# Performance work log

Hardware: AMD Instinct MI355X
Metric: run time of the kernel (lower is better)

## Reference

```python
import jax, jax.numpy as jnp
import numpy as np

N_NODES = 3070
N_FEAT = 128
N_OUT = 64
H_SIZE = 50
N_EDGES = 49120
BATCH = 128


def setup_inputs() -> dict:
    key = jax.random.key(0)
    ks = jax.random.split(key, 8)
    x_in = jax.random.normal(ks[0], (BATCH, N_NODES, N_FEAT), dtype=jnp.float32)
    edge_index = jax.random.randint(ks[1], (2, N_EDGES), 0, N_NODES, dtype=jnp.int64)
    edge_weight = jax.random.uniform(ks[2], (N_EDGES,), dtype=jnp.float32)
    W = jax.random.normal(ks[3], (N_FEAT, N_OUT), dtype=jnp.float32) / np.sqrt(N_FEAT)
    b = jnp.zeros((N_OUT,), dtype=jnp.float32)
    W_ih = jax.random.normal(ks[4], (H_SIZE, N_OUT), dtype=jnp.float32) / np.sqrt(N_OUT)
    W_hh = jax.random.normal(ks[5], (H_SIZE, H_SIZE), dtype=jnp.float32) / np.sqrt(H_SIZE)
    b_ih = jnp.zeros((H_SIZE,), dtype=jnp.float32)
    b_hh = jnp.zeros((H_SIZE,), dtype=jnp.float32)
    h0 = jax.random.normal(ks[6], (N_NODES, H_SIZE), dtype=jnp.float32)
    return {"x_in": x_in, "edge_index": edge_index, "edge_weight": edge_weight,
            "W": W, "b": b, "W_ih": W_ih, "W_hh": W_hh, "b_ih": b_ih,
            "b_hh": b_hh, "h0": h0}


def _gcn(x, edge_index, edge_weight, W, b):
    # x: (B, N, F). Vectorized GCNConv over the per-sample python loop.
    n = x.shape[1]
    # vectorized form of the dict-based edge-id remap: rank among unique ids
    uniq = jnp.unique(edge_index, size=n, fill_value=2 ** 30)
    ei = jnp.searchsorted(uniq, edge_index)
    src, dst = ei[0], ei[1]
    # GCNConv default: add self loops with weight 1, symmetric normalization
    loop = jnp.arange(n)
    src = jnp.concatenate([src, loop])
    dst = jnp.concatenate([dst, loop])
    ew = jnp.concatenate([edge_weight, jnp.ones((n,), dtype=x.dtype)])
    deg = jax.ops.segment_sum(ew, dst, num_segments=n)
    dinv = jnp.where(deg > 0, jax.lax.rsqrt(deg), jnp.zeros_like(deg))
    norm = dinv[src] * ew * dinv[dst]                 # (E+N,)
    xw = jnp.einsum('bnf,fo->bno', x, W)              # transform first
    msg = xw[:, src, :] * norm[None, :, None]         # (B, E+N, O)
    out = jnp.zeros_like(xw).at[:, dst, :].add(msg)   # scatter-add to targets
    return out + b


def reference(x_in, edge_index, edge_weight, W, b, W_ih, W_hh, b_ih, b_hh, h0):
    # GCN over all B graph samples (shared fixed graph)
    x = _gcn(x_in, edge_index, edge_weight, W, b)     # (B, N, O)
    # input_horizon==3 -> exactly one horizon step; the torch RNN is seq-first,
    # so seq_len = B (sample dim) and batch = N_NODES, hidden hardcoded 50.
    def step(h, xt):                                   # xt: (N, O), h: (N, H)
        h = jnp.tanh(xt @ W_ih.T + b_ih + h @ W_hh.T + b_hh)
        return h, h
    _, x_out = jax.lax.scan(step, h0, x)               # (B, N, H)
    return x_out
```

## Files before the change

kernel.cpp:

```cpp
#include <hip/hip_runtime.h>

#define NN 3070
#define NF 128
#define NO 64
#define NH 50
#define NC 52
#define NE 49120
#define NB 128
#define MTOT (NB * NN)
#define GCAP 1024
#define NBLK 192
#define GWG (NBLK * NB)
#define GPX (GWG / 8)

__global__ __launch_bounds__(256) void init_kernel(int* __restrict__ zb,
    const float* __restrict__ W, const float* __restrict__ Wih, const float* __restrict__ b,
    const float* __restrict__ bih, const float* __restrict__ bhh,
    float* __restrict__ Wp, float* __restrict__ bp) {
  int blk = blockIdx.x;
  int tid = threadIdx.x;
  if (blk < 48) {
    int i = blk * 256 + tid;
    if (i < 4 * NN) zb[i] = 0;
    return;
  }
  int idx = (blk - 48) * 256 + tid;
  if (idx < 128 * 64) {
    int k = idx >> 6, j = idx & 63;
    float s = 0.f;
    if (j < NH) {
      for (int o = 0; o < NO; ++o) s += W[k * NO + o] * Wih[j * NO + o];
    }
    Wp[k * 64 + j] = s;
  }
  if (idx < NC) {
    float s = 0.f;
    if (idx < NH) {
      for (int o = 0; o < NO; ++o) s += b[o] * Wih[idx * NO + o];
      s += bih[idx] + bhh[idx];
    }
    bp[idx] = s;
  }
}

__global__ __launch_bounds__(256) void mark_kernel(const int* __restrict__ ei, int* __restrict__ mark) {
  int i = blockIdx.x * 256 + threadIdx.x;
  if (i < 2 * NE) mark[ei[i]] = 1;
}

__global__ __launch_bounds__(1024) void exscan_kernel(const int* __restrict__ in, int* __restrict__ out,
                                                      int n, int write_total, int do_dinv,
                                                      const float* __restrict__ degw,
                                                      float* __restrict__ dinv, float* __restrict__ selfn) {
  __shared__ int part[1024];
  int tid = threadIdx.x;
  int base = tid * 3;
  if (do_dinv) {
#pragma unroll
    for (int u = 0; u < 3; ++u) {
      int nd = base + u;
      if (nd < NN) {
        float dg = degw[nd] + 1.0f;
        float di = rsqrtf(dg);
        dinv[nd] = di;
        selfn[nd] = di * di;
      }
    }
  }
  int v0 = (base + 0 < n) ? in[base + 0] : 0;
  int v1 = (base + 1 < n) ? in[base + 1] : 0;
  int v2 = (base + 2 < n) ? in[base + 2] : 0;
  int s = v0 + v1 + v2;
  part[tid] = s;
  __syncthreads();
  for (int off = 1; off < 1024; off <<= 1) {
    int t = (tid >= off) ? part[tid - off] : 0;
    __syncthreads();
    part[tid] += t;
    __syncthreads();
  }
  int run = part[tid] - s;
  if (base + 0 < n) out[base + 0] = run; run += v0;
  if (base + 1 < n) out[base + 1] = run; run += v1;
  if (base + 2 < n) out[base + 2] = run;
  if (write_total && tid == 1023) out[n] = part[1023];
}

__global__ __launch_bounds__(256) void remap_deg_kernel(const int* __restrict__ ei, const float* __restrict__ ew,
    const int* __restrict__ ranks, int* __restrict__ srcr, int* __restrict__ dstr,
    int* __restrict__ degc, float* __restrict__ degw) {
  int e = blockIdx.x * 256 + threadIdx.x;
  if (e >= NE) return;
  int s = ranks[ei[e]];
  int d = ranks[ei[NE + e]];
  srcr[e] = s;
  dstr[e] = d;
  atomicAdd(&degc[d], 1);
  atomicAdd(&degw[d], ew[e]);
}

__global__ __launch_bounds__(256) void csr_fill_kernel(const float* __restrict__ ew, const int* __restrict__ srcr,
    const int* __restrict__ dstr, const int* __restrict__ rowptr, int* __restrict__ cursor,
    const float* __restrict__ dinv, int* __restrict__ csr_src, float* __restrict__ csr_norm) {
  int e = blockIdx.x * 256 + threadIdx.x;
  if (e >= NE) return;
  int d = dstr[e];
  int s = srcr[e];
  int pos = rowptr[d] + atomicAdd(&cursor[d], 1);
  csr_src[pos] = s;
  csr_norm[pos] = dinv[s] * ew[e] * dinv[d];
}

__global__ __launch_bounds__(256, 3) void gemm_kernel(const float* __restrict__ A,
    const float* __restrict__ W, float* __restrict__ out) {
  __shared__ float As[256 * 36];
  __shared__ float Ws[32 * 64];
  int tid = threadIdx.x;
  int row0 = blockIdx.x * 256;
  int rg = tid >> 3;
  int cg = tid & 7;
  int c0 = cg * 8;
  float acc[8][8];
#pragma unroll
  for (int i = 0; i < 8; ++i)
#pragma unroll
    for (int j = 0; j < 8; ++j) acc[i][j] = 0.f;

  for (int kc = 0; kc < 4; ++kc) {
#pragma unroll
    for (int j = 0; j < 8; ++j) {
      int f = tid + 256 * j;
      int r = f >> 3, kq = f & 7;
      float4 v = *(const float4*)&A[(size_t)(row0 + r) * NF + kc * 32 + kq * 4];
      *(float4*)&As[r * 36 + kq * 4] = v;
    }
#pragma unroll
    for (int j = 0; j < 2; ++j) {
      int f = tid + 256 * j;
      int kk = f >> 4, cq = f & 15;
      *(float4*)&Ws[kk * 64 + cq * 4] = *(const float4*)&W[(size_t)(kc * 32 + kk) * 64 + cq * 4];
    }
    __syncthreads();
#pragma unroll 2
    for (int k4 = 0; k4 < 32; k4 += 4) {
      float4 a[8];
#pragma unroll
      for (int i = 0; i < 8; ++i) a[i] = *(const float4*)&As[(rg + 32 * i) * 36 + k4];
#pragma unroll
      for (int m = 0; m < 4; ++m) {
        float4 w0 = *(const float4*)&Ws[(k4 + m) * 64 + c0];
        float4 w1 = *(const float4*)&Ws[(k4 + m) * 64 + c0 + 4];
#pragma unroll
        for (int i = 0; i < 8; ++i) {
          float av = (m == 0) ? a[i].x : (m == 1) ? a[i].y : (m == 2) ? a[i].z : a[i].w;
          acc[i][0] += av * w0.x; acc[i][1] += av * w0.y;
          acc[i][2] += av * w0.z; acc[i][3] += av * w0.w;
          acc[i][4] += av * w1.x; acc[i][5] += av * w1.y;
          acc[i][6] += av * w1.z; acc[i][7] += av * w1.w;
        }
      }
    }
    __syncthreads();
  }
#pragma unroll
  for (int i = 0; i < 8; ++i) {
    size_t r = row0 + rg + 32 * i;
    if (c0 < NC)
      *(float4*)&out[r * NC + c0] = make_float4(acc[i][0], acc[i][1], acc[i][2], acc[i][3]);
    if (c0 + 4 < NC)
      *(float4*)&out[r * NC + c0 + 4] = make_float4(acc[i][4], acc[i][5], acc[i][6], acc[i][7]);
  }
}

__global__ __launch_bounds__(256) void gather_kernel(const float4* __restrict__ xw,
    const int* __restrict__ rowptr, const int* __restrict__ csr_src, const float* __restrict__ csr_norm,
    const float* __restrict__ selfn, const float* __restrict__ bp, float4* __restrict__ outg) {
  __shared__ int s_src[GCAP];
  __shared__ float s_nrm[GCAP];
  int bid = blockIdx.x;
  int xcd = bid & 7;
  int pos = bid >> 3;
  int work = xcd * GPX + pos;
  int b = work / NBLK;
  int nblk = work - b * NBLK;
  int tid = threadIdx.x;
  int f4 = tid & 15, nl = tid >> 4;
  int nb = nblk * 16;
  int nend = nb + 16 < NN ? nb + 16 : NN;
  int be0 = rowptr[nb], be1 = rowptr[nend];
  int cnt = be1 - be0;
  int scnt = cnt < GCAP ? cnt : GCAP;
  for (int i = tid; i < scnt; i += 256) {
    s_src[i] = csr_src[be0 + i];
    s_nrm[i] = csr_norm[be0 + i];
  }
  __syncthreads();
  int n = nb + nl;
  if (n >= NN || f4 >= 13) return;
  const float4* xb = xw + (size_t)b * NN * 13;
  float sn = selfn[n];
  float4 v = xb[n * 13 + f4];
  float ax = v.x * sn, ay = v.y * sn, az = v.z * sn, aw = v.w * sn;
  float bx = 0.f, by = 0.f, bz = 0.f, bw = 0.f;
  int le0 = rowptr[n] - be0, le1 = rowptr[n + 1] - be0;
  int lim = le1 < GCAP ? le1 : GCAP;
  int e = le0;
  for (; e + 1 < lim; e += 2) {
    int s1 = s_src[e], s2 = s_src[e + 1];
    float w1 = s_nrm[e], w2 = s_nrm[e + 1];
    float4 u1 = xb[s1 * 13 + f4];
    float4 u2 = xb[s2 * 13 + f4];
    ax += w1 * u1.x; ay += w1 * u1.y; az += w1 * u1.z; aw += w1 * u1.w;
    bx += w2 * u2.x; by += w2 * u2.y; bz += w2 * u2.z; bw += w2 * u2.w;
  }
  if (e < lim) {
    int s1 = s_src[e];
    float w1 = s_nrm[e];
    float4 u1 = xb[s1 * 13 + f4];
    ax += w1 * u1.x; ay += w1 * u1.y; az += w1 * u1.z; aw += w1 * u1.w;
  }
  for (e = (le0 > GCAP ? le0 : GCAP); e < le1; ++e) {
    int s1 = csr_src[be0 + e];
    float w1 = csr_norm[be0 + e];
    float4 u1 = xb[s1 * 13 + f4];
    ax += w1 * u1.x; ay += w1 * u1.y; az += w1 * u1.z; aw += w1 * u1.w;
  }
  float4 bb = ((const float4*)bp)[f4];
  float4 o = make_float4(ax + bx + bb.x, ay + by + bb.y, az + bz + bb.z, aw + bw + bb.w);
  outg[((size_t)b * NN + n) * 13 + f4] = o;
}

__global__ __launch_bounds__(256, 3) void rnn_kernel(const float* __restrict__ pre,
    const float* __restrict__ Whh, const float* __restrict__ h0, float* __restrict__ out) {
  __shared__ float hs[2][6 * 52];
  int tid = threadIdx.x;
  int n0 = blockIdx.x * 5;
  int nl = tid / 50;
  int j = tid - nl * 50;
  bool active = tid < 250;
  int jj = active ? j : 0;
  float2 whh2[25];
  const float2* whhp = (const float2*)(Whh + jj * NH);
#pragma unroll
  for (int q = 0; q < 25; ++q) whh2[q] = whhp[q];
  for (int i = tid; i < 2 * 6 * 52; i += 256) ((float*)hs)[i] = 0.f;
  __syncthreads();
  if (active) hs[0][nl * 52 + j] = h0[n0 * 50 + tid];
  const size_t NPRE = (size_t)NN * NC;
  const size_t NOUT = (size_t)NN * NH;
  int nn = active ? (n0 + nl) : n0;
  const float* prep = pre + (size_t)nn * NC + jj;
  float xp0 = prep[0];
  float xp1 = prep[NPRE];
  int widx = active ? (nl * 52 + j) : (5 * 52 + (tid - 250));
  __syncthreads();
#pragma unroll 2
  for (int t = 0; t < NB; ++t) {
    float a0 = xp0, a1 = 0.f, a2 = 0.f, a3 = 0.f;
    xp0 = xp1;
    if (t + 2 < NB) xp1 = prep[(size_t)(t + 2) * NPRE];
    const float* hb = hs[t & 1];
    const float4* hr = (const float4*)&hb[nl * 52];
#pragma unroll
    for (int q = 0; q < 12; q += 4) {
      float4 h0v = hr[q], h1v = hr[q + 1], h2v = hr[q + 2], h3v = hr[q + 3];
      a0 += h0v.x * whh2[2*q].x   + h0v.y * whh2[2*q].y   + h0v.z * whh2[2*q+1].x + h0v.w * whh2[2*q+1].y;
      a1 += h1v.x * whh2[2*q+2].x + h1v.y * whh2[2*q+2].y + h1v.z * whh2[2*q+3].x + h1v.w * whh2[2*q+3].y;
      a2 += h2v.x * whh2[2*q+4].x + h2v.y * whh2[2*q+4].y + h2v.z * whh2[2*q+5].x + h2v.w * whh2[2*q+5].y;
      a3 += h3v.x * whh2[2*q+6].x + h3v.y * whh2[2*q+6].y + h3v.z * whh2[2*q+7].x + h3v.w * whh2[2*q+7].y;
    }
    {
      float2 ht = *(const float2*)&hb[nl * 52 + 48];
      a0 += ht.x * whh2[24].x + ht.y * whh2[24].y;
    }
    float v = (a0 + a1) + (a2 + a3);
    float e = __expf(-2.f * fabsf(v));
    float r = (1.f - e) * __builtin_amdgcn_rcpf(1.f + e);
    float hnew = (v < 0.f) ? -r : r;
    hs[(t + 1) & 1][widx] = hnew;
    if (active) out[(size_t)t * NOUT + n0 * 50 + tid] = hnew;
    asm volatile("s_waitcnt lgkmcnt(0)" ::: "memory");
    __builtin_amdgcn_s_barrier();
  }
}


extern "C" void kernel_launch(void* const* d_in, const int* in_sizes, int n_in,
                              void* d_out, int out_size, void* d_ws, size_t ws_size,
                              hipStream_t stream) {
  const float* x_in = (const float*)d_in[0];
  const int* ei     = (const int*)d_in[1];
  const float* ew   = (const float*)d_in[2];
  const float* W    = (const float*)d_in[3];
  const float* bias = (const float*)d_in[4];
  const float* Wih  = (const float*)d_in[5];
  const float* Whh  = (const float*)d_in[6];
  const float* bih  = (const float*)d_in[7];
  const float* bhh  = (const float*)d_in[8];
  const float* h0   = (const float*)d_in[9];
  float* out = (float*)d_out;

  char* ws = (char*)d_ws;
  size_t off = 0;
  auto alloc = [&](size_t bytes) {
    size_t o = off;
    off += (bytes + 255) & ~(size_t)255;
    return o;
  };
  float* xw    = (float*)(ws + alloc((size_t)MTOT * NC * 4));
  float* gcn   = (float*)(ws + alloc((size_t)MTOT * NC * 4));
  int*   zb    = (int*)(ws + alloc((size_t)4 * NN * 4));
  int* mark = zb;
  int* degc = zb + NN;
  float* degw = (float*)(zb + 2 * NN);
  int* cursor = zb + 3 * NN;
  int*   ranks  = (int*)(ws + alloc(NN * 4));
  int*   srcr   = (int*)(ws + alloc(NE * 4));
  int*   dstr   = (int*)(ws + alloc(NE * 4));
  float* dinv   = (float*)(ws + alloc(NN * 4));
  float* selfn  = (float*)(ws + alloc(NN * 4));
  int*   rowptr = (int*)(ws + alloc((NN + 1) * 4));
  int*   csrc   = (int*)(ws + alloc(NE * 4));
  float* cnorm  = (float*)(ws + alloc(NE * 4));
  float* Wp     = (float*)(ws + alloc(128 * 64 * 4));
  float* bp     = (float*)(ws + alloc(NC * 4));

  init_kernel<<<80, 256, 0, stream>>>(zb, W, Wih, bias, bih, bhh, Wp, bp);
  mark_kernel<<<(2 * NE + 255) / 256, 256, 0, stream>>>(ei, mark);
  exscan_kernel<<<1, 1024, 0, stream>>>(mark, ranks, NN, 0, 0, degw, dinv, selfn);
  remap_deg_kernel<<<(NE + 255) / 256, 256, 0, stream>>>(ei, ew, ranks, srcr, dstr, degc, degw);
  exscan_kernel<<<1, 1024, 0, stream>>>(degc, rowptr, NN, 1, 1, degw, dinv, selfn);
  csr_fill_kernel<<<(NE + 255) / 256, 256, 0, stream>>>(ew, srcr, dstr, rowptr, cursor, dinv, csrc, cnorm);

  gemm_kernel<<<MTOT / 256, 256, 0, stream>>>(x_in, Wp, xw);
  gather_kernel<<<GWG, 256, 0, stream>>>(
      (const float4*)xw, rowptr, csrc, cnorm, selfn, bp, (float4*)gcn);
  rnn_kernel<<<(NN + 4) / 5, 256, 0, stream>>>(gcn, Whh, h0, out);
}
```

Measured before the change: 539.7 us.

## Map one RNN node per wavefront and drop block barriers

The recurrent kernel now gives each 64-lane wavefront one node instead of packing five nodes across a 256-thread block. This lets the hidden state live in a single shared-memory slot per wave, with no double buffering and no per-timestep block barrier. It relies on lanes in a wave executing in lockstep so the hidden-state reads finish before the writes. The input prefetch depth drops from two timesteps to one, and 14 of every 64 lanes sit idle.

After: 533.9 us. About the same (-1.1%).

```diff
diff --git a/kernel.cpp b/kernel.cpp
--- a/kernel.cpp
+++ b/kernel.cpp
@@ -232,35 +232,27 @@
 
 __global__ __launch_bounds__(256, 3) void rnn_kernel(const float* __restrict__ pre,
     const float* __restrict__ Whh, const float* __restrict__ h0, float* __restrict__ out) {
-  __shared__ float hs[2][6 * 52];
-  int tid = threadIdx.x;
-  int n0 = blockIdx.x * 5;
-  int nl = tid / 50;
-  int j = tid - nl * 50;
-  bool active = tid < 250;
+  __shared__ float hs[4 * 64];
+  int tid = threadIdx.x;
+  int w = tid >> 6;
+  int j = tid & 63;
+  int n = blockIdx.x * 4 + w;
+  if (n >= NN) return;
+  bool active = j < NH;
   int jj = active ? j : 0;
   float2 whh2[25];
   const float2* whhp = (const float2*)(Whh + jj * NH);
 #pragma unroll
   for (int q = 0; q < 25; ++q) whh2[q] = whhp[q];
-  for (int i = tid; i < 2 * 6 * 52; i += 256) ((float*)hs)[i] = 0.f;
-  __syncthreads();
-  if (active) hs[0][nl * 52 + j] = h0[n0 * 50 + tid];
+  hs[w * 64 + j] = active ? h0[(size_t)n * NH + j] : 0.f;
   const size_t NPRE = (size_t)NN * NC;
   const size_t NOUT = (size_t)NN * NH;
-  int nn = active ? (n0 + nl) : n0;
-  const float* prep = pre + (size_t)nn * NC + jj;
-  float xp0 = prep[0];
-  float xp1 = prep[NPRE];
-  int widx = active ? (nl * 52 + j) : (5 * 52 + (tid - 250));
-  __syncthreads();
-#pragma unroll 2
+  const float* prep = pre + (size_t)n * NC + jj;
+  float xpre = prep[0];
+  const float4* hr = (const float4*)&hs[w * 64];
   for (int t = 0; t < NB; ++t) {
-    float a0 = xp0, a1 = 0.f, a2 = 0.f, a3 = 0.f;
-    xp0 = xp1;
-    if (t + 2 < NB) xp1 = prep[(size_t)(t + 2) * NPRE];
-    const float* hb = hs[t & 1];
-    const float4* hr = (const float4*)&hb[nl * 52];
+    float a0 = xpre, a1 = 0.f, a2 = 0.f, a3 = 0.f;
+    if (t + 1 < NB) xpre = prep[(size_t)(t + 1) * NPRE];
 #pragma unroll
     for (int q = 0; q < 12; q += 4) {
       float4 h0v = hr[q], h1v = hr[q + 1], h2v = hr[q + 2], h3v = hr[q + 3];
@@ -270,17 +262,17 @@
       a3 += h3v.x * whh2[2*q+6].x + h3v.y * whh2[2*q+6].y + h3v.z * whh2[2*q+7].x + h3v.w * whh2[2*q+7].y;
     }
     {
-      float2 ht = *(const float2*)&hb[nl * 52 + 48];
+      float2 ht = *(const float2*)&hs[w * 64 + 48];
       a0 += ht.x * whh2[24].x + ht.y * whh2[24].y;
     }
     float v = (a0 + a1) + (a2 + a3);
     float e = __expf(-2.f * fabsf(v));
     float r = (1.f - e) * __builtin_amdgcn_rcpf(1.f + e);
     float hnew = (v < 0.f) ? -r : r;
-    hs[(t + 1) & 1][widx] = hnew;
-    if (active) out[(size_t)t * NOUT + n0 * 50 + tid] = hnew;
-    asm volatile("s_waitcnt lgkmcnt(0)" ::: "memory");
-    __builtin_amdgcn_s_barrier();
+    if (active) {
+      hs[w * 64 + j] = hnew;
+      out[(size_t)t * NOUT + (size_t)n * NH + j] = hnew;
+    }
   }
 }
 
@@ -335,5 +327,5 @@
   gemm_kernel<<<MTOT / 256, 256, 0, stream>>>(x_in, Wp, xw);
   gather_kernel<<<GWG, 256, 0, stream>>>(
       (const float4*)xw, rowptr, csrc, cnorm, selfn, bp, (float4*)gcn);
-  rnn_kernel<<<(NN + 4) / 5, 256, 0, stream>>>(gcn, Whh, h0, out);
-}
+  rnn_kernel<<<(NN + 3) / 4, 256, 0, stream>>>(gcn, Whh, h0, out);
+}
```
